# Kernel tuning notes

Measured on AMD Instinct MI355X. Metric: run time of the kernel, lower is better.

The kernel has to match this reference:

```python
import jax, jax.numpy as jnp
import numpy as np
import math

D_MODEL = 1024
H = 16
D_K = D_MODEL // H
D_FF = 4096
EPS = 1e-6


def layer_norm(x, gamma, beta):
    # torch LayerNorm-variant: unbiased std, eps added to std (not var)
    mean = jnp.mean(x, axis=-1, keepdims=True)
    std = jnp.std(x, axis=-1, keepdims=True, ddof=1)
    return gamma * (x - mean) / (std + EPS) + beta


def mha(x, mask, w_q, w_k, w_v, w_o):
    B, S, _ = x.shape
    # torch Linear (no bias): y = x @ W.T
    q = (x @ w_q.T).reshape(B, S, H, D_K).transpose(0, 2, 1, 3)
    k = (x @ w_k.T).reshape(B, S, H, D_K).transpose(0, 2, 1, 3)
    v = (x @ w_v.T).reshape(B, S, H, D_K).transpose(0, 2, 1, 3)
    scores = jnp.einsum('bhqd,bhkd->bhqk', q, k) / math.sqrt(D_K)
    scores = jnp.where(mask == 0, jnp.float32(-1e9), scores)
    attn = jax.nn.softmax(scores, axis=-1)
    out = jnp.einsum('bhqk,bhkd->bhqd', attn, v)
    out = out.transpose(0, 2, 1, 3).reshape(B, S, D_MODEL)
    return out @ w_o.T


def setup_inputs() -> dict:
    key = jax.random.key(0)
    ks = jax.random.split(key, 12)
    B, S = 4, 2048
    s = 0.02
    return {
        'x': jax.random.normal(ks[0], (B, S, D_MODEL), jnp.float32),
        'src_mask': jnp.ones((B, 1, 1, S), jnp.int32),
        'w_q': jax.random.normal(ks[1], (D_MODEL, D_MODEL), jnp.float32) * s,
        'w_k': jax.random.normal(ks[2], (D_MODEL, D_MODEL), jnp.float32) * s,
        'w_v': jax.random.normal(ks[3], (D_MODEL, D_MODEL), jnp.float32) * s,
        'w_o': jax.random.normal(ks[4], (D_MODEL, D_MODEL), jnp.float32) * s,
        'w1': jax.random.normal(ks[5], (D_FF, D_MODEL), jnp.float32) * s,
        'b1': jnp.zeros((D_FF,), jnp.float32),
        'w2': jax.random.normal(ks[6], (D_MODEL, D_FF), jnp.float32) * s,
        'b2': jnp.zeros((D_MODEL,), jnp.float32),
        'gamma1': jnp.ones((D_MODEL,), jnp.float32),
        'beta1': jnp.zeros((D_MODEL,), jnp.float32),
        'gamma2': jnp.ones((D_MODEL,), jnp.float32),
        'beta2': jnp.zeros((D_MODEL,), jnp.float32),
    }


def reference(x, src_mask, w_q, w_k, w_v, w_o, w1, b1, w2, b2,
              gamma1, beta1, gamma2, beta2):
    # AddNorm1: x + MHA(LN(x))  (pre-norm, dropout=0)
    x = x + mha(layer_norm(x, gamma1, beta1), src_mask, w_q, w_k, w_v, w_o)
    # AddNorm2: x + FFN(LN(x))
    h = layer_norm(x, gamma2, beta2)
    ffn = jax.nn.relu(h @ w1.T + b1) @ w2.T + b2
    return x + ffn
```

## Files before the change

kernel.cpp:

```cpp
#include <hip/hip_runtime.h>

#define D_MODEL 1024
#define NH 16
#define DK 64
#define DFF 4096
#define SEQ 2048
#define BATCH 4
#define NROWS (BATCH*SEQ)
#define CHUNK 2048
#define NCHUNK (NROWS/CHUNK)

typedef short bf16x8 __attribute__((ext_vector_type(8)));
typedef float f32x4 __attribute__((ext_vector_type(4)));

__device__ __forceinline__ float bf2f(unsigned short u){
  union { float f; unsigned int i; } x; x.i = ((unsigned int)u) << 16; return x.f;
}
__device__ __forceinline__ unsigned short f2bf(float f){
  union { float f; unsigned int i; } x; x.f = f;
  unsigned int r = x.i + 0x7fffu + ((x.i >> 16) & 1u);
  return (unsigned short)(r >> 16);
}
__device__ __forceinline__ float fexp2(float x){
#if __has_builtin(__builtin_amdgcn_exp2f)
  return __builtin_amdgcn_exp2f(x);
#else
  return __exp2f(x);
#endif
}

__device__ __forceinline__ void gl_lds16(const void* g, void* l) {
  __builtin_amdgcn_global_load_lds((const __attribute__((address_space(1))) void*)g,
                                   (__attribute__((address_space(3))) void*)l, 16, 0, 0);
}

__global__ __launch_bounds__(256) void cvt_f2b(const float* __restrict__ in,
                                               unsigned short* __restrict__ out, int n)
{
  int i = (blockIdx.x * 256 + threadIdx.x) * 4;
  if (i < n) {
    float4 f = *(const float4*)(in + i);
    union { int2 v; unsigned short u[4]; } o;
    o.u[0] = f2bf(f.x); o.u[1] = f2bf(f.y); o.u[2] = f2bf(f.z); o.u[3] = f2bf(f.w);
    *(int2*)(out + i) = o.v;
  }
}

__global__ __launch_bounds__(256) void ln_kernel(const float* __restrict__ in,
    const float* __restrict__ gam, const float* __restrict__ bet,
    unsigned short* __restrict__ out)
{
  const int row = blockIdx.x, t = threadIdx.x;
  const int base = t * 4;
  float4 raw = *(const float4*)(in + (size_t)row * D_MODEL + base);
  float v[4] = { raw.x, raw.y, raw.z, raw.w };
  float s  = v[0] + v[1] + v[2] + v[3];
  float s2 = v[0]*v[0] + v[1]*v[1] + v[2]*v[2] + v[3]*v[3];
  #pragma unroll
  for (int off = 32; off > 0; off >>= 1) {
    s  += __shfl_down(s,  off);
    s2 += __shfl_down(s2, off);
  }
  __shared__ float red[10];
  const int wid = t >> 6, lane = t & 63;
  if (lane == 0) { red[wid] = s; red[4 + wid] = s2; }
  __syncthreads();
  if (t == 0) {
    float ts  = red[0] + red[1] + red[2] + red[3];
    float ts2 = red[4] + red[5] + red[6] + red[7];
    float mean = ts * (1.0f / D_MODEL);
    float var  = (ts2 - (float)D_MODEL * mean * mean) * (1.0f / (D_MODEL - 1));
    var = fmaxf(var, 0.0f);
    red[8] = mean;
    red[9] = 1.0f / (sqrtf(var) + 1e-6f);
  }
  __syncthreads();
  const float mean = red[8], inv = red[9];
  float4 g4 = *(const float4*)(gam + base);
  float4 b4 = *(const float4*)(bet + base);
  union { int2 v; unsigned short u[4]; } o;
  o.u[0] = f2bf(g4.x * (v[0] - mean) * inv + b4.x);
  o.u[1] = f2bf(g4.y * (v[1] - mean) * inv + b4.y);
  o.u[2] = f2bf(g4.z * (v[2] - mean) * inv + b4.z);
  o.u[3] = f2bf(g4.w * (v[3] - mean) * inv + b4.w);
  *(int2*)(out + (size_t)row * D_MODEL + base) = o.v;
}

__global__ __launch_bounds__(256) void gemm_bt(
    const unsigned short* __restrict__ A,
    const unsigned short* __restrict__ Bw,
    int K, int N, int sA, int sB,
    const float* __restrict__ bias,
    int relu,
    const float* __restrict__ residf,
    unsigned short* __restrict__ outb,
    float* __restrict__ outf,
    float* __restrict__ atomf,
    unsigned short* __restrict__ outq,
    unsigned short* __restrict__ outk,
    unsigned short* __restrict__ outvt)
{
  __shared__ __attribute__((aligned(16))) short sAm[128 * 32];
  __shared__ __attribute__((aligned(16))) short sBm[128 * 32];
  const int t = threadIdx.x;
  const int tileN = blockIdx.x * 128;
  const int tileM = blockIdx.y * 128;
  const int kz = blockIdx.z;
  const size_t koff = (size_t)kz * K;
  const int wid = t >> 6, lane = t & 63;
  const int wM = (wid >> 1) * 64, wN = (wid & 1) * 64;
  const int quad = lane >> 4, lrow = lane & 15;

  f32x4 acc[4][4] = {};

  for (int k0 = 0; k0 < K; k0 += 32) {
    #pragma unroll
    for (int it = 0; it < 2; it++) {
      int seg = it * 256 + t;
      int row = seg >> 2, c8 = (seg & 3) * 8;
      gl_lds16(A  + (size_t)(tileM + row) * sA + koff + k0 + c8, &sAm[seg * 8]);
      gl_lds16(Bw + (size_t)(tileN + row) * sB + koff + k0 + c8, &sBm[seg * 8]);
    }
    __syncthreads();
    bf16x8 af[4], bfr[4];
    #pragma unroll
    for (int i = 0; i < 4; i++) {
      af[i]  = *(const bf16x8*)&sAm[(wM + i * 16 + lrow) * 32 + quad * 8];
      bfr[i] = *(const bf16x8*)&sBm[(wN + i * 16 + lrow) * 32 + quad * 8];
    }
    #pragma unroll
    for (int i = 0; i < 4; i++)
      #pragma unroll
      for (int j = 0; j < 4; j++)
        acc[i][j] = __builtin_amdgcn_mfma_f32_16x16x32_bf16(af[i], bfr[j], acc[i][j], 0, 0, 0);
    __syncthreads();
  }

  unsigned short* qk_out = nullptr;
  int qkv_cat = 0;
  if (outq) {
    qkv_cat = tileN >> 10;
    qk_out = (qkv_cat == 0) ? outq : outk;
  }

  #pragma unroll
  for (int i = 0; i < 4; i++) {
    #pragma unroll
    for (int j = 0; j < 4; j++) {
      const int col  = tileN + wN + j * 16 + lrow;
      const int row0 = tileM + wM + i * 16 + quad * 4;
      const float bv = (bias && kz == 0) ? bias[col] : 0.0f;
      float vals[4];
      #pragma unroll
      for (int r = 0; r < 4; r++) {
        float val = acc[i][j][r] + bv;
        if (relu) val = fmaxf(val, 0.0f);
        if (residf) val += residf[(size_t)(row0 + r) * N + col];
        vals[r] = val;
      }
      if (outq) {
        const int lcol = col & 1023;
        if (qkv_cat < 2) {
          #pragma unroll
          for (int r = 0; r < 4; r++)
            qk_out[(size_t)(row0 + r) * D_MODEL + lcol] = f2bf(vals[r]);
        } else {
          union { int2 v; unsigned short u[4]; } pk;
          #pragma unroll
          for (int r = 0; r < 4; r++) pk.u[r] = f2bf(vals[r]);
          size_t tidx = (((size_t)(row0 >> 11) * NH + (lcol >> 6)) * DK + (lcol & 63)) * SEQ + (row0 & 2047);
          *(int2*)(outvt + tidx) = pk.v;
        }
      } else if (atomf) {
        #pragma unroll
        for (int r = 0; r < 4; r++)
          atomicAdd(&atomf[(size_t)(row0 + r) * N + col], vals[r]);
      } else {
        #pragma unroll
        for (int r = 0; r < 4; r++) {
          const size_t idx = (size_t)(row0 + r) * N + col;
          if (outf) outf[idx] = vals[r];
          if (outb) outb[idx] = f2bf(vals[r]);
        }
      }
    }
  }
}

#define AQT 64
#define AKT 64
__global__ __launch_bounds__(256) void attn_mfma(
    const unsigned short* __restrict__ Qg,
    const unsigned short* __restrict__ Kg,
    const unsigned short* __restrict__ Vt,
    const int* __restrict__ mask,
    unsigned short* __restrict__ Og)
{
  __shared__ __attribute__((aligned(16))) short Ks[AKT * 64];
  __shared__ __attribute__((aligned(16))) short Vs[DK * 64];
  __shared__ __attribute__((aligned(16))) short Ps[AQT * 64];
  __shared__ __attribute__((aligned(16))) float maddf[AKT];

  const int bid = blockIdx.x;
  const int nqt = SEQ / AQT;
  const int b  = bid / (NH * nqt);
  const int h  = (bid / nqt) % NH;
  const int q0 = (bid % nqt) * AQT;
  const int t  = threadIdx.x;
  const int wv = t >> 6, lane = t & 63;
  const int quad = lane >> 4, l15 = lane & 15;
  const int sw = (l15 & 7) << 3;
  const float SCL = 0.125f * 1.44269504f;

  bf16x8 qf0, qf1;
  {
    const unsigned short* qrow = Qg + (size_t)(b * SEQ + q0 + wv * 16 + l15) * D_MODEL + h * DK;
    qf0 = *(const bf16x8*)(qrow + quad * 8);
    qf1 = *(const bf16x8*)(qrow + 32 + quad * 8);
  }
  f32x4 oacc[4] = {};
  float m_run = -1e30f, l_run = 0.0f;

  const unsigned short* Kbase = Kg + (size_t)(b * SEQ) * D_MODEL + h * DK;
  const unsigned short* Vbase = Vt + ((size_t)(b * NH + h) * DK) * SEQ;

  for (int kt = 0; kt < SEQ; kt += AKT) {
    #pragma unroll
    for (int it = 0; it < 2; it++) {
      int s = it * 256 + t;
      int row = s >> 3;
      int scol = ((s & 7) * 8) ^ ((row & 7) << 3);
      gl_lds16(Kbase + (size_t)(kt + row) * D_MODEL + scol, &Ks[s * 8]);
      gl_lds16(Vbase + (size_t)row * SEQ + kt + scol, &Vs[s * 8]);
    }
    if (t < AKT) maddf[t] = mask[b * SEQ + kt + t] ? 0.0f : -1.0e9f;
    __syncthreads();

    f32x4 sc[4];
    #pragma unroll
    for (int ct = 0; ct < 4; ct++) {
      const int krow = ct * 16 + l15;
      bf16x8 kb0 = *(const bf16x8*)&Ks[krow * 64 + ((quad * 8) ^ sw)];
      bf16x8 kb1 = *(const bf16x8*)&Ks[krow * 64 + ((32 + quad * 8) ^ sw)];
      f32x4 a = {};
      a = __builtin_amdgcn_mfma_f32_16x16x32_bf16(kb0, qf0, a, 0, 0, 0);
      a = __builtin_amdgcn_mfma_f32_16x16x32_bf16(kb1, qf1, a, 0, 0, 0);
      f32x4 md = *(const f32x4*)&maddf[ct * 16 + quad * 4];
      #pragma unroll
      for (int r = 0; r < 4; r++) a[r] = a[r] * SCL + md[r];
      sc[ct] = a;
    }

    float tmax = sc[0][0];
    #pragma unroll
    for (int ct = 0; ct < 4; ct++)
      #pragma unroll
      for (int r = 0; r < 4; r++) tmax = fmaxf(tmax, sc[ct][r]);
    tmax = fmaxf(tmax, __shfl_xor(tmax, 16));
    tmax = fmaxf(tmax, __shfl_xor(tmax, 32));

    if (!__all(tmax - m_run <= 11.5415603f)) {
      float mn = fmaxf(m_run, tmax);
      float alpha = fexp2(m_run - mn);
      m_run = mn;
      l_run *= alpha;
      float a4[4];
      #pragma unroll
      for (int r = 0; r < 4; r++) a4[r] = __shfl(alpha, quad * 4 + r);
      #pragma unroll
      for (int dt = 0; dt < 4; dt++)
        #pragma unroll
        for (int r = 0; r < 4; r++) oacc[dt][r] *= a4[r];
    }

    const int prow = wv * 16 + l15;
    float rs = 0.0f;
    #pragma unroll
    for (int ct = 0; ct < 4; ct++) {
      float p0 = fexp2(sc[ct][0] - m_run);
      float p1 = fexp2(sc[ct][1] - m_run);
      float p2 = fexp2(sc[ct][2] - m_run);
      float p3 = fexp2(sc[ct][3] - m_run);
      rs += (p0 + p1) + (p2 + p3);
      unsigned int lo, hi;
      asm("v_cvt_pk_bf16_f32 %0, %1, %2" : "=v"(lo) : "v"(p0), "v"(p1));
      asm("v_cvt_pk_bf16_f32 %0, %1, %2" : "=v"(hi) : "v"(p2), "v"(p3));
      int2 pv; pv.x = (int)lo; pv.y = (int)hi;
      *(int2*)&Ps[prow * 64 + ((ct * 16 + quad * 4) ^ sw)] = pv;
    }
    rs += __shfl_xor(rs, 16);
    rs += __shfl_xor(rs, 32);
    l_run += rs;

    bf16x8 pf0 = *(const bf16x8*)&Ps[prow * 64 + ((quad * 8) ^ sw)];
    bf16x8 pf1 = *(const bf16x8*)&Ps[prow * 64 + ((32 + quad * 8) ^ sw)];
    #pragma unroll
    for (int dt = 0; dt < 4; dt++) {
      const int vrow = dt * 16 + l15;
      bf16x8 vb0 = *(const bf16x8*)&Vs[vrow * 64 + ((quad * 8) ^ sw)];
      bf16x8 vb1 = *(const bf16x8*)&Vs[vrow * 64 + ((32 + quad * 8) ^ sw)];
      oacc[dt] = __builtin_amdgcn_mfma_f32_16x16x32_bf16(pf0, vb0, oacc[dt], 0, 0, 0);
      oacc[dt] = __builtin_amdgcn_mfma_f32_16x16x32_bf16(pf1, vb1, oacc[dt], 0, 0, 0);
    }
    __syncthreads();
  }

  float li = 1.0f / l_run;
  float linv4[4];
  #pragma unroll
  for (int r = 0; r < 4; r++) linv4[r] = __shfl(li, quad * 4 + r);
  #pragma unroll
  for (int dt = 0; dt < 4; dt++)
    #pragma unroll
    for (int r = 0; r < 4; r++)
      Og[(size_t)(b * SEQ + q0 + wv * 16 + quad * 4 + r) * D_MODEL + h * DK + dt * 16 + l15] =
        f2bf(oacc[dt][r] * linv4[r]);
}

extern "C" void kernel_launch(void* const* d_in, const int* in_sizes, int n_in,
                              void* d_out, int out_size, void* d_ws, size_t ws_size,
                              hipStream_t stream)
{
  (void)in_sizes; (void)n_in; (void)out_size; (void)ws_size;
  const float* x   = (const float*)d_in[0];
  const int*   msk = (const int*)d_in[1];
  const float* w_q = (const float*)d_in[2];
  const float* w_k = (const float*)d_in[3];
  const float* w_v = (const float*)d_in[4];
  const float* w_o = (const float*)d_in[5];
  const float* w1  = (const float*)d_in[6];
  const float* b1  = (const float*)d_in[7];
  const float* w2  = (const float*)d_in[8];
  const float* b2  = (const float*)d_in[9];
  const float* g1  = (const float*)d_in[10];
  const float* be1 = (const float*)d_in[11];
  const float* g2  = (const float*)d_in[12];
  const float* be2 = (const float*)d_in[13];
  float* outf = (float*)d_out;

  char* ws = (char*)d_ws;
  const size_t MB = 1024 * 1024;
  unsigned short* q_b  = (unsigned short*)(ws + 0);
  unsigned short* k_b  = (unsigned short*)(ws + 16 * MB);
  unsigned short* vt_b = (unsigned short*)(ws + 32 * MB);
  unsigned short* wo16 = (unsigned short*)(ws + 16 * MB);
  unsigned short* w116 = (unsigned short*)(ws + 0);
  unsigned short* w216 = (unsigned short*)(ws + 8 * MB);
  unsigned short* ln2b = vt_b;
  unsigned short* hffc = k_b;

  unsigned short* ln1b   = (unsigned short*)d_out;
  unsigned short* wqkv16 = (unsigned short*)d_out + 8 * 1024 * 1024;

  dim3 blk(256);
  const int nw = D_MODEL * D_MODEL;
  const int nf = DFF * D_MODEL;

  cvt_f2b<<<nw / 1024, blk, 0, stream>>>(w_q, wqkv16, nw);
  cvt_f2b<<<nw / 1024, blk, 0, stream>>>(w_k, wqkv16 + nw, nw);
  cvt_f2b<<<nw / 1024, blk, 0, stream>>>(w_v, wqkv16 + 2 * nw, nw);
  ln_kernel<<<NROWS, blk, 0, stream>>>(x, g1, be1, ln1b);

  dim3 gqkv(3 * D_MODEL / 128, NROWS / 128);
  gemm_bt<<<gqkv, blk, 0, stream>>>(ln1b, wqkv16, D_MODEL, 3 * D_MODEL, D_MODEL, D_MODEL,
                                    nullptr, 0, nullptr, nullptr, nullptr, nullptr,
                                    q_b, k_b, vt_b);

  attn_mfma<<<BATCH * NH * (SEQ / AQT), blk, 0, stream>>>(q_b, k_b, vt_b, msk, q_b);

  cvt_f2b<<<nw / 1024, blk, 0, stream>>>(w_o, wo16, nw);
  dim3 gN1024(D_MODEL / 128, NROWS / 128);
  gemm_bt<<<gN1024, blk, 0, stream>>>(q_b, wo16, D_MODEL, D_MODEL, D_MODEL, D_MODEL,
                                      nullptr, 0, x, nullptr, outf, nullptr,
                                      nullptr, nullptr, nullptr);

  cvt_f2b<<<nf / 1024, blk, 0, stream>>>(w1, w116, nf);
  cvt_f2b<<<nf / 1024, blk, 0, stream>>>(w2, w216, nf);
  ln_kernel<<<NROWS, blk, 0, stream>>>(outf, g2, be2, ln2b);
  for (int c = 0; c < NCHUNK; c++) {
    const size_t ro = (size_t)c * CHUNK;
    dim3 g1c(DFF / 128,     CHUNK / 128);
    dim3 g2c(D_MODEL / 128, CHUNK / 128, 4);
    gemm_bt<<<g1c, blk, 0, stream>>>(ln2b + ro * D_MODEL, w116, D_MODEL, DFF,
                                     D_MODEL, D_MODEL, b1, 1,
                                     nullptr, hffc, nullptr, nullptr,
                                     nullptr, nullptr, nullptr);
    gemm_bt<<<g2c, blk, 0, stream>>>(hffc, w216, DFF / 4, D_MODEL, DFF, DFF, b2, 0,
                                     nullptr, nullptr, nullptr, outf + ro * D_MODEL,
                                     nullptr, nullptr, nullptr);
  }
}
```

Measured before the change: 774.3 us.

## Double-buffer LDS tiles in GEMM and attention kernels to overlap loads

Result: faster. 727.2 us (-6.1%).

```diff
diff --git a/kernel.cpp b/kernel.cpp
--- a/kernel.cpp
+++ b/kernel.cpp
@@ -100,8 +100,10 @@
     unsigned short* __restrict__ outk,
     unsigned short* __restrict__ outvt)
 {
-  __shared__ __attribute__((aligned(16))) short sAm[128 * 32];
-  __shared__ __attribute__((aligned(16))) short sBm[128 * 32];
+  __shared__ __attribute__((aligned(16))) short sA0[128 * 32];
+  __shared__ __attribute__((aligned(16))) short sA1[128 * 32];
+  __shared__ __attribute__((aligned(16))) short sB0[128 * 32];
+  __shared__ __attribute__((aligned(16))) short sB1[128 * 32];
   const int t = threadIdx.x;
   const int tileN = blockIdx.x * 128;
   const int tileM = blockIdx.y * 128;
@@ -113,26 +115,38 @@
 
   f32x4 acc[4][4] = {};
 
-  for (int k0 = 0; k0 < K; k0 += 32) {
-    #pragma unroll
-    for (int it = 0; it < 2; it++) {
-      int seg = it * 256 + t;
+  auto stage = [&](short* dA, short* dB, int k0) {
+    #pragma unroll
+    for (int it2 = 0; it2 < 2; it2++) {
+      int seg = it2 * 256 + t;
       int row = seg >> 2, c8 = (seg & 3) * 8;
-      gl_lds16(A  + (size_t)(tileM + row) * sA + koff + k0 + c8, &sAm[seg * 8]);
-      gl_lds16(Bw + (size_t)(tileN + row) * sB + koff + k0 + c8, &sBm[seg * 8]);
-    }
-    __syncthreads();
+      gl_lds16(A  + (size_t)(tileM + row) * sA + koff + k0 + c8, dA + seg * 8);
+      gl_lds16(Bw + (size_t)(tileN + row) * sB + koff + k0 + c8, dB + seg * 8);
+    }
+  };
+  auto compute = [&](const short* cA, const short* cB) {
     bf16x8 af[4], bfr[4];
     #pragma unroll
     for (int i = 0; i < 4; i++) {
-      af[i]  = *(const bf16x8*)&sAm[(wM + i * 16 + lrow) * 32 + quad * 8];
-      bfr[i] = *(const bf16x8*)&sBm[(wN + i * 16 + lrow) * 32 + quad * 8];
+      af[i]  = *(const bf16x8*)&cA[(wM + i * 16 + lrow) * 32 + quad * 8];
+      bfr[i] = *(const bf16x8*)&cB[(wN + i * 16 + lrow) * 32 + quad * 8];
     }
     #pragma unroll
     for (int i = 0; i < 4; i++)
       #pragma unroll
       for (int j = 0; j < 4; j++)
         acc[i][j] = __builtin_amdgcn_mfma_f32_16x16x32_bf16(af[i], bfr[j], acc[i][j], 0, 0, 0);
+  };
+
+  const int nk = K >> 5;
+  stage(sA0, sB0, 0);
+  __syncthreads();
+  for (int ik = 0; ik < nk; ik += 2) {
+    if (ik + 1 < nk) stage(sA1, sB1, (ik + 1) << 5);
+    compute(sA0, sB0);
+    __syncthreads();
+    if (ik + 2 < nk) stage(sA0, sB0, (ik + 2) << 5);
+    compute(sA1, sB1);
     __syncthreads();
   }
 
@@ -196,10 +210,13 @@
     const int* __restrict__ mask,
     unsigned short* __restrict__ Og)
 {
-  __shared__ __attribute__((aligned(16))) short Ks[AKT * 64];
-  __shared__ __attribute__((aligned(16))) short Vs[DK * 64];
-  __shared__ __attribute__((aligned(16))) short Ps[AQT * 64];
-  __shared__ __attribute__((aligned(16))) float maddf[AKT];
+  __shared__ __attribute__((aligned(16))) short Ks0[AKT * 64];
+  __shared__ __attribute__((aligned(16))) short Ks1[AKT * 64];
+  __shared__ __attribute__((aligned(16))) short Vs0[DK * 64];
+  __shared__ __attribute__((aligned(16))) short Vs1[DK * 64];
+  __shared__ __attribute__((aligned(16))) short Psm[AQT * 64];
+  __shared__ __attribute__((aligned(16))) float mf0[AKT];
+  __shared__ __attribute__((aligned(16))) float mf1[AKT];
 
   const int bid = blockIdx.x;
   const int nqt = SEQ / AQT;
@@ -224,28 +241,29 @@
   const unsigned short* Kbase = Kg + (size_t)(b * SEQ) * D_MODEL + h * DK;
   const unsigned short* Vbase = Vt + ((size_t)(b * NH + h) * DK) * SEQ;
 
-  for (int kt = 0; kt < SEQ; kt += AKT) {
-    #pragma unroll
-    for (int it = 0; it < 2; it++) {
-      int s = it * 256 + t;
+  auto stageKV = [&](short* kd, short* vd, float* mf, int kt) {
+    #pragma unroll
+    for (int it2 = 0; it2 < 2; it2++) {
+      int s = it2 * 256 + t;
       int row = s >> 3;
       int scol = ((s & 7) * 8) ^ ((row & 7) << 3);
-      gl_lds16(Kbase + (size_t)(kt + row) * D_MODEL + scol, &Ks[s * 8]);
-      gl_lds16(Vbase + (size_t)row * SEQ + kt + scol, &Vs[s * 8]);
-    }
-    if (t < AKT) maddf[t] = mask[b * SEQ + kt + t] ? 0.0f : -1.0e9f;
-    __syncthreads();
-
+      gl_lds16(Kbase + (size_t)(kt + row) * D_MODEL + scol, kd + s * 8);
+      gl_lds16(Vbase + (size_t)row * SEQ + kt + scol, vd + s * 8);
+    }
+    if (t < AKT) mf[t] = mask[b * SEQ + kt + t] ? 0.0f : -1.0e9f;
+  };
+
+  auto tilecomp = [&](const short* Ksc, const short* Vsc, const float* mfc) {
     f32x4 sc[4];
     #pragma unroll
     for (int ct = 0; ct < 4; ct++) {
       const int krow = ct * 16 + l15;
-      bf16x8 kb0 = *(const bf16x8*)&Ks[krow * 64 + ((quad * 8) ^ sw)];
-      bf16x8 kb1 = *(const bf16x8*)&Ks[krow * 64 + ((32 + quad * 8) ^ sw)];
+      bf16x8 kb0 = *(const bf16x8*)&Ksc[krow * 64 + ((quad * 8) ^ sw)];
+      bf16x8 kb1 = *(const bf16x8*)&Ksc[krow * 64 + ((32 + quad * 8) ^ sw)];
       f32x4 a = {};
       a = __builtin_amdgcn_mfma_f32_16x16x32_bf16(kb0, qf0, a, 0, 0, 0);
       a = __builtin_amdgcn_mfma_f32_16x16x32_bf16(kb1, qf1, a, 0, 0, 0);
-      f32x4 md = *(const f32x4*)&maddf[ct * 16 + quad * 4];
+      f32x4 md = *(const f32x4*)&mfc[ct * 16 + quad * 4];
       #pragma unroll
       for (int r = 0; r < 4; r++) a[r] = a[r] * SCL + md[r];
       sc[ct] = a;
@@ -286,22 +304,33 @@
       asm("v_cvt_pk_bf16_f32 %0, %1, %2" : "=v"(lo) : "v"(p0), "v"(p1));
       asm("v_cvt_pk_bf16_f32 %0, %1, %2" : "=v"(hi) : "v"(p2), "v"(p3));
       int2 pv; pv.x = (int)lo; pv.y = (int)hi;
-      *(int2*)&Ps[prow * 64 + ((ct * 16 + quad * 4) ^ sw)] = pv;
+      *(int2*)&Psm[prow * 64 + ((ct * 16 + quad * 4) ^ sw)] = pv;
     }
     rs += __shfl_xor(rs, 16);
     rs += __shfl_xor(rs, 32);
     l_run += rs;
 
-    bf16x8 pf0 = *(const bf16x8*)&Ps[prow * 64 + ((quad * 8) ^ sw)];
-    bf16x8 pf1 = *(const bf16x8*)&Ps[prow * 64 + ((32 + quad * 8) ^ sw)];
+    bf16x8 pf0 = *(const bf16x8*)&Psm[prow * 64 + ((quad * 8) ^ sw)];
+    bf16x8 pf1 = *(const bf16x8*)&Psm[prow * 64 + ((32 + quad * 8) ^ sw)];
     #pragma unroll
     for (int dt = 0; dt < 4; dt++) {
       const int vrow = dt * 16 + l15;
-      bf16x8 vb0 = *(const bf16x8*)&Vs[vrow * 64 + ((quad * 8) ^ sw)];
-      bf16x8 vb1 = *(const bf16x8*)&Vs[vrow * 64 + ((32 + quad * 8) ^ sw)];
+      bf16x8 vb0 = *(const bf16x8*)&Vsc[vrow * 64 + ((quad * 8) ^ sw)];
+      bf16x8 vb1 = *(const bf16x8*)&Vsc[vrow * 64 + ((32 + quad * 8) ^ sw)];
       oacc[dt] = __builtin_amdgcn_mfma_f32_16x16x32_bf16(pf0, vb0, oacc[dt], 0, 0, 0);
       oacc[dt] = __builtin_amdgcn_mfma_f32_16x16x32_bf16(pf1, vb1, oacc[dt], 0, 0, 0);
     }
+  };
+
+  stageKV(Ks0, Vs0, mf0, 0);
+  __syncthreads();
+  for (int it = 0; it < SEQ / AKT; it += 2) {
+    const int kt = it * AKT;
+    if (it + 1 < SEQ / AKT) stageKV(Ks1, Vs1, mf1, kt + AKT);
+    tilecomp(Ks0, Vs0, mf0);
+    __syncthreads();
+    if (it + 2 < SEQ / AKT) stageKV(Ks0, Vs0, mf0, kt + 2 * AKT);
+    tilecomp(Ks1, Vs1, mf1);
     __syncthreads();
   }
 
```

## Double-buffer GEMM LDS tiles and process two query groups per attention block

Applied to the files above, without the earlier changes.

New measurement: 707.2 us. 1.09x faster.

```diff
diff --git a/kernel.cpp b/kernel.cpp
--- a/kernel.cpp
+++ b/kernel.cpp
@@ -100,8 +100,10 @@
     unsigned short* __restrict__ outk,
     unsigned short* __restrict__ outvt)
 {
-  __shared__ __attribute__((aligned(16))) short sAm[128 * 32];
-  __shared__ __attribute__((aligned(16))) short sBm[128 * 32];
+  __shared__ __attribute__((aligned(16))) short sA0[128 * 32];
+  __shared__ __attribute__((aligned(16))) short sA1[128 * 32];
+  __shared__ __attribute__((aligned(16))) short sB0[128 * 32];
+  __shared__ __attribute__((aligned(16))) short sB1[128 * 32];
   const int t = threadIdx.x;
   const int tileN = blockIdx.x * 128;
   const int tileM = blockIdx.y * 128;
@@ -113,26 +115,45 @@
 
   f32x4 acc[4][4] = {};
 
-  for (int k0 = 0; k0 < K; k0 += 32) {
-    #pragma unroll
-    for (int it = 0; it < 2; it++) {
-      int seg = it * 256 + t;
-      int row = seg >> 2, c8 = (seg & 3) * 8;
-      gl_lds16(A  + (size_t)(tileM + row) * sA + koff + k0 + c8, &sAm[seg * 8]);
-      gl_lds16(Bw + (size_t)(tileN + row) * sB + koff + k0 + c8, &sBm[seg * 8]);
-    }
-    __syncthreads();
+  const unsigned short* pa = A  + (size_t)(tileM + (t >> 2)) * sA + koff + (t & 3) * 8;
+  const unsigned short* pb = Bw + (size_t)(tileN + (t >> 2)) * sB + koff + (t & 3) * 8;
+  const size_t a64 = (size_t)64 * sA, b64 = (size_t)64 * sB;
+
+  auto stage = [&]() {
+    gl_lds16(pa,       0 + t * 8 + (short*)nullptr);
+  };
+  (void)stage;
+
+  auto stageTo = [&](short* dA, short* dB) {
+    gl_lds16(pa,       dA + t * 8);
+    gl_lds16(pa + a64, dA + (256 + t) * 8);
+    gl_lds16(pb,       dB + t * 8);
+    gl_lds16(pb + b64, dB + (256 + t) * 8);
+    pa += 32; pb += 32;
+  };
+  auto compute = [&](const short* cA, const short* cB) {
     bf16x8 af[4], bfr[4];
     #pragma unroll
     for (int i = 0; i < 4; i++) {
-      af[i]  = *(const bf16x8*)&sAm[(wM + i * 16 + lrow) * 32 + quad * 8];
-      bfr[i] = *(const bf16x8*)&sBm[(wN + i * 16 + lrow) * 32 + quad * 8];
+      af[i]  = *(const bf16x8*)&cA[(wM + i * 16 + lrow) * 32 + quad * 8];
+      bfr[i] = *(const bf16x8*)&cB[(wN + i * 16 + lrow) * 32 + quad * 8];
     }
     #pragma unroll
     for (int i = 0; i < 4; i++)
       #pragma unroll
       for (int j = 0; j < 4; j++)
         acc[i][j] = __builtin_amdgcn_mfma_f32_16x16x32_bf16(af[i], bfr[j], acc[i][j], 0, 0, 0);
+  };
+
+  const int nk = K >> 5;
+  stageTo(sA0, sB0);
+  __syncthreads();
+  for (int ik = 0; ik < nk; ik += 2) {
+    if (ik + 1 < nk) stageTo(sA1, sB1);
+    compute(sA0, sB0);
+    __syncthreads();
+    if (ik + 2 < nk) stageTo(sA0, sB0);
+    compute(sA1, sB1);
     __syncthreads();
   }
 
@@ -187,7 +208,7 @@
   }
 }
 
-#define AQT 64
+#define AQT 128
 #define AKT 64
 __global__ __launch_bounds__(256) void attn_mfma(
     const unsigned short* __restrict__ Qg,
@@ -198,7 +219,7 @@
 {
   __shared__ __attribute__((aligned(16))) short Ks[AKT * 64];
   __shared__ __attribute__((aligned(16))) short Vs[DK * 64];
-  __shared__ __attribute__((aligned(16))) short Ps[AQT * 64];
+  __shared__ __attribute__((aligned(16))) short Ps[64 * 64];
   __shared__ __attribute__((aligned(16))) float maddf[AKT];
 
   const int bid = blockIdx.x;
@@ -212,109 +233,117 @@
   const int sw = (l15 & 7) << 3;
   const float SCL = 0.125f * 1.44269504f;
 
-  bf16x8 qf0, qf1;
-  {
-    const unsigned short* qrow = Qg + (size_t)(b * SEQ + q0 + wv * 16 + l15) * D_MODEL + h * DK;
-    qf0 = *(const bf16x8*)(qrow + quad * 8);
-    qf1 = *(const bf16x8*)(qrow + 32 + quad * 8);
-  }
-  f32x4 oacc[4] = {};
-  float m_run = -1e30f, l_run = 0.0f;
-
-  const unsigned short* Kbase = Kg + (size_t)(b * SEQ) * D_MODEL + h * DK;
-  const unsigned short* Vbase = Vt + ((size_t)(b * NH + h) * DK) * SEQ;
+  bf16x8 qf[2][2];
+  #pragma unroll
+  for (int g = 0; g < 2; g++) {
+    const unsigned short* qrow =
+        Qg + (size_t)(b * SEQ + q0 + g * 64 + wv * 16 + l15) * D_MODEL + h * DK;
+    qf[g][0] = *(const bf16x8*)(qrow + quad * 8);
+    qf[g][1] = *(const bf16x8*)(qrow + 32 + quad * 8);
+  }
+  f32x4 oacc[2][4] = {};
+  float m_run[2] = { -1e30f, -1e30f };
+  float l_run[2] = { 0.0f, 0.0f };
+
+  const int srow = t >> 3;
+  const int scol = ((t & 7) * 8) ^ ((srow & 7) << 3);
+  const unsigned short* kp = Kg + (size_t)(b * SEQ + srow) * D_MODEL + h * DK + scol;
+  const unsigned short* vp = Vt + ((size_t)(b * NH + h) * DK + srow) * SEQ + scol;
+  const int* mp = mask + b * SEQ;
+  const int prow = wv * 16 + l15;
 
   for (int kt = 0; kt < SEQ; kt += AKT) {
-    #pragma unroll
-    for (int it = 0; it < 2; it++) {
-      int s = it * 256 + t;
-      int row = s >> 3;
-      int scol = ((s & 7) * 8) ^ ((row & 7) << 3);
-      gl_lds16(Kbase + (size_t)(kt + row) * D_MODEL + scol, &Ks[s * 8]);
-      gl_lds16(Vbase + (size_t)row * SEQ + kt + scol, &Vs[s * 8]);
-    }
-    if (t < AKT) maddf[t] = mask[b * SEQ + kt + t] ? 0.0f : -1.0e9f;
+    gl_lds16(kp,                  &Ks[t * 8]);
+    gl_lds16(kp + 32 * D_MODEL,   &Ks[(256 + t) * 8]);
+    gl_lds16(vp,                  &Vs[t * 8]);
+    gl_lds16(vp + 32 * SEQ,       &Vs[(256 + t) * 8]);
+    if (t < AKT) maddf[t] = mp[t] ? 0.0f : -1.0e9f;
     __syncthreads();
 
-    f32x4 sc[4];
-    #pragma unroll
-    for (int ct = 0; ct < 4; ct++) {
-      const int krow = ct * 16 + l15;
-      bf16x8 kb0 = *(const bf16x8*)&Ks[krow * 64 + ((quad * 8) ^ sw)];
-      bf16x8 kb1 = *(const bf16x8*)&Ks[krow * 64 + ((32 + quad * 8) ^ sw)];
-      f32x4 a = {};
-      a = __builtin_amdgcn_mfma_f32_16x16x32_bf16(kb0, qf0, a, 0, 0, 0);
-      a = __builtin_amdgcn_mfma_f32_16x16x32_bf16(kb1, qf1, a, 0, 0, 0);
-      f32x4 md = *(const f32x4*)&maddf[ct * 16 + quad * 4];
-      #pragma unroll
-      for (int r = 0; r < 4; r++) a[r] = a[r] * SCL + md[r];
-      sc[ct] = a;
-    }
-
-    float tmax = sc[0][0];
-    #pragma unroll
-    for (int ct = 0; ct < 4; ct++)
-      #pragma unroll
-      for (int r = 0; r < 4; r++) tmax = fmaxf(tmax, sc[ct][r]);
-    tmax = fmaxf(tmax, __shfl_xor(tmax, 16));
-    tmax = fmaxf(tmax, __shfl_xor(tmax, 32));
-
-    if (!__all(tmax - m_run <= 11.5415603f)) {
-      float mn = fmaxf(m_run, tmax);
-      float alpha = fexp2(m_run - mn);
-      m_run = mn;
-      l_run *= alpha;
-      float a4[4];
-      #pragma unroll
-      for (int r = 0; r < 4; r++) a4[r] = __shfl(alpha, quad * 4 + r);
-      #pragma unroll
-      for (int dt = 0; dt < 4; dt++)
+    #pragma unroll
+    for (int g = 0; g < 2; g++) {
+      f32x4 sc[4];
+      #pragma unroll
+      for (int ct = 0; ct < 4; ct++) {
+        const int krow = ct * 16 + l15;
+        bf16x8 kb0 = *(const bf16x8*)&Ks[krow * 64 + ((quad * 8) ^ sw)];
+        bf16x8 kb1 = *(const bf16x8*)&Ks[krow * 64 + ((32 + quad * 8) ^ sw)];
+        f32x4 a = {};
+        a = __builtin_amdgcn_mfma_f32_16x16x32_bf16(kb0, qf[g][0], a, 0, 0, 0);
+        a = __builtin_amdgcn_mfma_f32_16x16x32_bf16(kb1, qf[g][1], a, 0, 0, 0);
+        f32x4 md = *(const f32x4*)&maddf[ct * 16 + quad * 4];
         #pragma unroll
-        for (int r = 0; r < 4; r++) oacc[dt][r] *= a4[r];
-    }
-
-    const int prow = wv * 16 + l15;
-    float rs = 0.0f;
-    #pragma unroll
-    for (int ct = 0; ct < 4; ct++) {
-      float p0 = fexp2(sc[ct][0] - m_run);
-      float p1 = fexp2(sc[ct][1] - m_run);
-      float p2 = fexp2(sc[ct][2] - m_run);
-      float p3 = fexp2(sc[ct][3] - m_run);
-      rs += (p0 + p1) + (p2 + p3);
-      unsigned int lo, hi;
-      asm("v_cvt_pk_bf16_f32 %0, %1, %2" : "=v"(lo) : "v"(p0), "v"(p1));
-      asm("v_cvt_pk_bf16_f32 %0, %1, %2" : "=v"(hi) : "v"(p2), "v"(p3));
-      int2 pv; pv.x = (int)lo; pv.y = (int)hi;
-      *(int2*)&Ps[prow * 64 + ((ct * 16 + quad * 4) ^ sw)] = pv;
-    }
-    rs += __shfl_xor(rs, 16);
-    rs += __shfl_xor(rs, 32);
-    l_run += rs;
-
-    bf16x8 pf0 = *(const bf16x8*)&Ps[prow * 64 + ((quad * 8) ^ sw)];
-    bf16x8 pf1 = *(const bf16x8*)&Ps[prow * 64 + ((32 + quad * 8) ^ sw)];
-    #pragma unroll
-    for (int dt = 0; dt < 4; dt++) {
-      const int vrow = dt * 16 + l15;
-      bf16x8 vb0 = *(const bf16x8*)&Vs[vrow * 64 + ((quad * 8) ^ sw)];
-      bf16x8 vb1 = *(const bf16x8*)&Vs[vrow * 64 + ((32 + quad * 8) ^ sw)];
-      oacc[dt] = __builtin_amdgcn_mfma_f32_16x16x32_bf16(pf0, vb0, oacc[dt], 0, 0, 0);
-      oacc[dt] = __builtin_amdgcn_mfma_f32_16x16x32_bf16(pf1, vb1, oacc[dt], 0, 0, 0);
+        for (int r = 0; r < 4; r++) a[r] = a[r] * SCL + md[r];
+        sc[ct] = a;
+      }
+
+      float tmax = fmaxf(fmaxf(sc[0][0], sc[0][1]), fmaxf(sc[0][2], sc[0][3]));
+      #pragma unroll
+      for (int ct = 1; ct < 4; ct++)
+        tmax = fmaxf(tmax, fmaxf(fmaxf(sc[ct][0], sc[ct][1]), fmaxf(sc[ct][2], sc[ct][3])));
+      tmax = fmaxf(tmax, __shfl_xor(tmax, 16));
+      tmax = fmaxf(tmax, __shfl_xor(tmax, 32));
+
+      if (!__all(tmax - m_run[g] <= 11.5415603f)) {
+        float mn = fmaxf(m_run[g], tmax);
+        float alpha = fexp2(m_run[g] - mn);
+        m_run[g] = mn;
+        l_run[g] *= alpha;
+        float a4[4];
+        #pragma unroll
+        for (int r = 0; r < 4; r++) a4[r] = __shfl(alpha, quad * 4 + r);
+        #pragma unroll
+        for (int dt = 0; dt < 4; dt++)
+          #pragma unroll
+          for (int r = 0; r < 4; r++) oacc[g][dt][r] *= a4[r];
+      }
+
+      float rs = 0.0f;
+      #pragma unroll
+      for (int ct = 0; ct < 4; ct++) {
+        float p0 = fexp2(sc[ct][0] - m_run[g]);
+        float p1 = fexp2(sc[ct][1] - m_run[g]);
+        float p2 = fexp2(sc[ct][2] - m_run[g]);
+        float p3 = fexp2(sc[ct][3] - m_run[g]);
+        rs += (p0 + p1) + (p2 + p3);
+        unsigned int lo, hi;
+        asm("v_cvt_pk_bf16_f32 %0, %1, %2" : "=v"(lo) : "v"(p0), "v"(p1));
+        asm("v_cvt_pk_bf16_f32 %0, %1, %2" : "=v"(hi) : "v"(p2), "v"(p3));
+        int2 pv; pv.x = (int)lo; pv.y = (int)hi;
+        *(int2*)&Ps[prow * 64 + ((ct * 16 + quad * 4) ^ sw)] = pv;
+      }
+      rs += __shfl_xor(rs, 16);
+      rs += __shfl_xor(rs, 32);
+      l_run[g] += rs;
+
+      bf16x8 pf0 = *(const bf16x8*)&Ps[prow * 64 + ((quad * 8) ^ sw)];
+      bf16x8 pf1 = *(const bf16x8*)&Ps[prow * 64 + ((32 + quad * 8) ^ sw)];
+      #pragma unroll
+      for (int dt = 0; dt < 4; dt++) {
+        const int vrow = dt * 16 + l15;
+        bf16x8 vb0 = *(const bf16x8*)&Vs[vrow * 64 + ((quad * 8) ^ sw)];
+        bf16x8 vb1 = *(const bf16x8*)&Vs[vrow * 64 + ((32 + quad * 8) ^ sw)];
+        oacc[g][dt] = __builtin_amdgcn_mfma_f32_16x16x32_bf16(pf0, vb0, oacc[g][dt], 0, 0, 0);
+        oacc[g][dt] = __builtin_amdgcn_mfma_f32_16x16x32_bf16(pf1, vb1, oacc[g][dt], 0, 0, 0);
+      }
     }
     __syncthreads();
-  }
-
-  float li = 1.0f / l_run;
-  float linv4[4];
+    kp += (size_t)AKT * D_MODEL; vp += AKT; mp += AKT;
+  }
+
   #pragma unroll
-  for (int r = 0; r < 4; r++) linv4[r] = __shfl(li, quad * 4 + r);
-  #pragma unroll
-  for (int dt = 0; dt < 4; dt++)
-    #pragma unroll
-    for (int r = 0; r < 4; r++)
-      Og[(size_t)(b * SEQ + q0 + wv * 16 + quad * 4 + r) * D_MODEL + h * DK + dt * 16 + l15] =
-        f2bf(oacc[dt][r] * linv4[r]);
+  for (int g = 0; g < 2; g++) {
+    float li = 1.0f / l_run[g];
+    float linv4[4];
+    #pragma unroll
+    for (int r = 0; r < 4; r++) linv4[r] = __shfl(li, quad * 4 + r);
+    #pragma unroll
+    for (int dt = 0; dt < 4; dt++)
+      #pragma unroll
+      for (int r = 0; r < 4; r++)
+        Og[(size_t)(b * SEQ + q0 + g * 64 + wv * 16 + quad * 4 + r) * D_MODEL + h * DK + dt * 16 + l15] =
+          f2bf(oacc[g][dt][r] * linv4[r]);
+  }
 }
 
 extern "C" void kernel_launch(void* const* d_in, const int* in_sizes, int n_in,
```
